# Optimization experiments

Measured on AMD Instinct MI355X. Metric: run time of the kernel, lower is better.

Reference implementation:

```python
import jax, jax.numpy as jnp
import numpy as np

N_WORDS = 100000
N_DIMS = 128
N = 65536
K = 10


def setup_inputs() -> dict:
    key = jax.random.key(0)
    k1, k2, k3, k4, k5 = jax.random.split(key, 5)
    input_idx = jax.random.randint(k1, (N,), 0, N_WORDS)
    output_idx = jax.random.randint(k2, (N,), 0, N_WORDS)
    neg_idx = jax.random.randint(k3, (N, K), 0, N_WORDS)
    # Embedding tables initialized uniform(-1, 1) as in the torch module
    W_in = jax.random.uniform(k4, (N_WORDS, N_DIMS), jnp.float32, -1.0, 1.0)
    W_out = jax.random.uniform(k5, (N_WORDS, N_DIMS), jnp.float32, -1.0, 1.0)
    return {"input_idx": input_idx, "output_idx": output_idx, "neg_idx": neg_idx,
            "W_in": W_in, "W_out": W_out}


def reference(input_idx, output_idx, neg_idx, W_in, W_out):
    in_vecs = W_in[input_idx]            # [N, D]
    out_vecs = W_out[output_idx]         # [N, D]
    neg_vecs = W_out[neg_idx]            # [N, K, D]
    prob = jnp.einsum('nd,nd->n', in_vecs, out_vecs)          # [N]
    noise = -jnp.einsum('nd,nkd->nk', in_vecs, neg_vecs)      # [N, K]
    loss = jnp.mean(jax.nn.log_sigmoid(prob) + jax.nn.log_sigmoid(noise).sum(axis=1))
    return loss
```

## Files before the change

### kernel.cpp

```cpp
#include <hip/hip_runtime.h>
#include <hip/hip_bf16.h>


#define N_SAMPLES 65536
#define N_DIMS 128
#define K_NEG 10

__global__ void zero_out_kernel(float* out) {
    if (threadIdx.x == 0 && blockIdx.x == 0) out[0] = 0.0f;
}

__device__ __forceinline__ float log_sigmoid_fast(float x) {
    float ax = fabsf(x);
    return fminf(x, 0.0f) - __logf(1.0f + __expf(-ax));
}

__device__ __forceinline__ float dot4(float4 a, float4 b) {
    return a.x * b.x + a.y * b.y + a.z * b.z + a.w * b.w;
}

__device__ __forceinline__ float group8_reduce(float v) {
    v += __shfl_xor(v, 4);
    v += __shfl_xor(v, 2);
    v += __shfl_xor(v, 1);
    return v;
}

__global__ __launch_bounds__(256, 2) void skipgram_kernel(
        const int* __restrict__ input_idx,
        const int* __restrict__ output_idx,
        const int* __restrict__ neg_idx,
        const float* __restrict__ W_in,
        const float* __restrict__ W_out,
        float* __restrict__ out)
{
    const int g = threadIdx.x & 7;
    const int n = (blockIdx.x * blockDim.x + threadIdx.x) >> 3;

    int idx[12];
    idx[0] = input_idx[n];
    idx[1] = output_idx[n];
    #pragma unroll
    for (int k = 0; k < K_NEG; ++k) idx[2 + k] = neg_idx[n * K_NEG + k];

    const float4* __restrict__ arow = (const float4*)(W_in + (size_t)idx[0] * N_DIMS);
    float4 a0 = arow[0 * 8 + g];
    float4 a1 = arow[1 * 8 + g];
    float4 a2 = arow[2 * 8 + g];
    float4 a3 = arow[3 * 8 + g];

    float4 r[11][4];
    #pragma unroll
    for (int t = 0; t < 11; ++t) {
        const float4* __restrict__ rr =
            (const float4*)(W_out + (size_t)idx[1 + t] * N_DIMS);
        r[t][0] = rr[0 * 8 + g];
        r[t][1] = rr[1 * 8 + g];
        r[t][2] = rr[2 * 8 + g];
        r[t][3] = rr[3 * 8 + g];
    }

    __builtin_amdgcn_sched_barrier(0);

    float acc = 0.0f;
    #pragma unroll
    for (int t = 0; t < 11; ++t) {
        float d = dot4(a0, r[t][0]) + dot4(a1, r[t][1])
                + dot4(a2, r[t][2]) + dot4(a3, r[t][3]);
        d = group8_reduce(d);
        acc += log_sigmoid_fast(t == 0 ? d : -d);
    }

    __shared__ float sdata[32];
    if (g == 0) sdata[threadIdx.x >> 3] = acc;
    __syncthreads();
    if (threadIdx.x < 32) {
        float s = sdata[threadIdx.x];
        s += __shfl_xor(s, 16);
        s += __shfl_xor(s, 8);
        s += __shfl_xor(s, 4);
        s += __shfl_xor(s, 2);
        s += __shfl_xor(s, 1);
        if (threadIdx.x == 0)
            atomicAdd(out, s * (1.0f / (float)N_SAMPLES));
    }
}

extern "C" void kernel_launch(void* const* d_in, const int* in_sizes, int n_in,
                              void* d_out, int out_size, void* d_ws, size_t ws_size,
                              hipStream_t stream) {
    const int*   input_idx  = (const int*)d_in[0];
    const int*   output_idx = (const int*)d_in[1];
    const int*   neg_idx    = (const int*)d_in[2];
    const float* W_in       = (const float*)d_in[3];
    const float* W_out      = (const float*)d_in[4];
    float* out = (float*)d_out;

    zero_out_kernel<<<1, 64, 0, stream>>>(out);

    const int block = 256;
    const int grid  = N_SAMPLES / (block / 8);
    skipgram_kernel<<<grid, block, 0, stream>>>(
        input_idx, output_idx, neg_idx, W_in, W_out, out);
}
```

Baseline: 158.6 us.

## Convert W_out to bf16 in workspace and gather half-width rows

Each call now runs a pre-pass that converts the whole W_out table to bf16 in the workspace buffer, and also zeroes the output. The main kernel then gathers 256-byte bf16 rows instead of 512-byte fp32 rows and widens them in registers before the dot products. This halves the bytes moved by the random-row gather, and the smaller register footprint allows an occupancy hint of 3. The trade-off is a full streaming read and write of the table on every call, plus some loss of precision in the W_out values. A fallback keeps the original fp32 path when the workspace is too small.

Result: no change. 155.6 us (-1.9%).

```diff
diff --git a/kernel.cpp b/kernel.cpp
--- a/kernel.cpp
+++ b/kernel.cpp
@@ -5,6 +5,8 @@
 #define N_SAMPLES 65536
 #define N_DIMS 128
 #define K_NEG 10
+#define N_WORDS 100000
+#define WOUT_BF16_BYTES ((size_t)N_WORDS * N_DIMS * 2)
 
 __global__ void zero_out_kernel(float* out) {
     if (threadIdx.x == 0 && blockIdx.x == 0) out[0] = 0.0f;
@@ -26,12 +28,59 @@
     return v;
 }
 
-__global__ __launch_bounds__(256, 2) void skipgram_kernel(
+__device__ __forceinline__ unsigned int f2bf(float f) {
+    unsigned int u = __float_as_uint(f);
+    return (u + 0x7FFFu + ((u >> 16) & 1u)) >> 16;
+}
+
+__global__ __launch_bounds__(256) void convert_kernel(
+        const float* __restrict__ W_out, unsigned int* __restrict__ dst,
+        float* __restrict__ out)
+{
+    if (blockIdx.x == 0 && threadIdx.x == 0) out[0] = 0.0f;
+    const size_t total8 = (size_t)N_WORDS * N_DIMS / 8;
+    const size_t stride = (size_t)gridDim.x * blockDim.x;
+    const float4* __restrict__ src = (const float4*)W_out;
+    for (size_t i = blockIdx.x * (size_t)blockDim.x + threadIdx.x;
+         i < total8; i += stride) {
+        float4 f0 = src[2 * i];
+        float4 f1 = src[2 * i + 1];
+        uint4 p;
+        p.x = f2bf(f0.x) | (f2bf(f0.y) << 16);
+        p.y = f2bf(f0.z) | (f2bf(f0.w) << 16);
+        p.z = f2bf(f1.x) | (f2bf(f1.y) << 16);
+        p.w = f2bf(f1.z) | (f2bf(f1.w) << 16);
+        ((uint4*)dst)[i] = p;
+    }
+}
+
+__device__ __forceinline__ float bflo(unsigned int u) {
+    return __uint_as_float(u << 16);
+}
+__device__ __forceinline__ float bfhi(unsigned int u) {
+    return __uint_as_float(u & 0xFFFF0000u);
+}
+__device__ __forceinline__ float dot_row_bf16(const float4 a0, const float4 a1,
+                                              const float4 a2, const float4 a3,
+                                              const uint4 b0, const uint4 b1) {
+    float acc;
+    acc  = a0.x * bflo(b0.x); acc = fmaf(a0.y, bfhi(b0.x), acc);
+    acc  = fmaf(a0.z, bflo(b0.y), acc); acc = fmaf(a0.w, bfhi(b0.y), acc);
+    acc  = fmaf(a1.x, bflo(b0.z), acc); acc = fmaf(a1.y, bfhi(b0.z), acc);
+    acc  = fmaf(a1.z, bflo(b0.w), acc); acc = fmaf(a1.w, bfhi(b0.w), acc);
+    acc  = fmaf(a2.x, bflo(b1.x), acc); acc = fmaf(a2.y, bfhi(b1.x), acc);
+    acc  = fmaf(a2.z, bflo(b1.y), acc); acc = fmaf(a2.w, bfhi(b1.y), acc);
+    acc  = fmaf(a3.x, bflo(b1.z), acc); acc = fmaf(a3.y, bfhi(b1.z), acc);
+    acc  = fmaf(a3.z, bflo(b1.w), acc); acc = fmaf(a3.w, bfhi(b1.w), acc);
+    return acc;
+}
+
+__global__ __launch_bounds__(256, 3) void skipgram_bf16_kernel(
         const int* __restrict__ input_idx,
         const int* __restrict__ output_idx,
         const int* __restrict__ neg_idx,
         const float* __restrict__ W_in,
-        const float* __restrict__ W_out,
+        const unsigned short* __restrict__ Wo16,
         float* __restrict__ out)
 {
     const int g = threadIdx.x & 7;
@@ -44,20 +93,18 @@
     for (int k = 0; k < K_NEG; ++k) idx[2 + k] = neg_idx[n * K_NEG + k];
 
     const float4* __restrict__ arow = (const float4*)(W_in + (size_t)idx[0] * N_DIMS);
-    float4 a0 = arow[0 * 8 + g];
-    float4 a1 = arow[1 * 8 + g];
-    float4 a2 = arow[2 * 8 + g];
-    float4 a3 = arow[3 * 8 + g];
-
-    float4 r[11][4];
-    #pragma unroll
-    for (int t = 0; t < 11; ++t) {
-        const float4* __restrict__ rr =
-            (const float4*)(W_out + (size_t)idx[1 + t] * N_DIMS);
-        r[t][0] = rr[0 * 8 + g];
-        r[t][1] = rr[1 * 8 + g];
-        r[t][2] = rr[2 * 8 + g];
-        r[t][3] = rr[3 * 8 + g];
+    float4 a0 = arow[4 * g + 0];
+    float4 a1 = arow[4 * g + 1];
+    float4 a2 = arow[4 * g + 2];
+    float4 a3 = arow[4 * g + 3];
+
+    uint4 r0[11], r1[11];
+    #pragma unroll
+    for (int t = 0; t < 11; ++t) {
+        const uint4* __restrict__ rr =
+            (const uint4*)(Wo16 + (size_t)idx[1 + t] * N_DIMS + 16 * g);
+        r0[t] = rr[0];
+        r1[t] = rr[1];
     }
 
     __builtin_amdgcn_sched_barrier(0);
@@ -65,8 +112,7 @@
     float acc = 0.0f;
     #pragma unroll
     for (int t = 0; t < 11; ++t) {
-        float d = dot4(a0, r[t][0]) + dot4(a1, r[t][1])
-                + dot4(a2, r[t][2]) + dot4(a3, r[t][3]);
+        float d = dot_row_bf16(a0, a1, a2, a3, r0[t], r1[t]);
         d = group8_reduce(d);
         acc += log_sigmoid_fast(t == 0 ? d : -d);
     }
@@ -86,6 +132,65 @@
     }
 }
 
+__global__ __launch_bounds__(256, 2) void skipgram_f32_kernel(
+        const int* __restrict__ input_idx,
+        const int* __restrict__ output_idx,
+        const int* __restrict__ neg_idx,
+        const float* __restrict__ W_in,
+        const float* __restrict__ W_out,
+        float* __restrict__ out)
+{
+    const int g = threadIdx.x & 7;
+    const int n = (blockIdx.x * blockDim.x + threadIdx.x) >> 3;
+
+    int idx[12];
+    idx[0] = input_idx[n];
+    idx[1] = output_idx[n];
+    #pragma unroll
+    for (int k = 0; k < K_NEG; ++k) idx[2 + k] = neg_idx[n * K_NEG + k];
+
+    const float4* __restrict__ arow = (const float4*)(W_in + (size_t)idx[0] * N_DIMS);
+    float4 a0 = arow[0 * 8 + g];
+    float4 a1 = arow[1 * 8 + g];
+    float4 a2 = arow[2 * 8 + g];
+    float4 a3 = arow[3 * 8 + g];
+
+    float4 r[11][4];
+    #pragma unroll
+    for (int t = 0; t < 11; ++t) {
+        const float4* __restrict__ rr =
+            (const float4*)(W_out + (size_t)idx[1 + t] * N_DIMS);
+        r[t][0] = rr[0 * 8 + g];
+        r[t][1] = rr[1 * 8 + g];
+        r[t][2] = rr[2 * 8 + g];
+        r[t][3] = rr[3 * 8 + g];
+    }
+    __builtin_amdgcn_sched_barrier(0);
+
+    float acc = 0.0f;
+    #pragma unroll
+    for (int t = 0; t < 11; ++t) {
+        float d = dot4(a0, r[t][0]) + dot4(a1, r[t][1])
+                + dot4(a2, r[t][2]) + dot4(a3, r[t][3]);
+        d = group8_reduce(d);
+        acc += log_sigmoid_fast(t == 0 ? d : -d);
+    }
+
+    __shared__ float sdata[32];
+    if (g == 0) sdata[threadIdx.x >> 3] = acc;
+    __syncthreads();
+    if (threadIdx.x < 32) {
+        float s = sdata[threadIdx.x];
+        s += __shfl_xor(s, 16);
+        s += __shfl_xor(s, 8);
+        s += __shfl_xor(s, 4);
+        s += __shfl_xor(s, 2);
+        s += __shfl_xor(s, 1);
+        if (threadIdx.x == 0)
+            atomicAdd(out, s * (1.0f / (float)N_SAMPLES));
+    }
+}
+
 extern "C" void kernel_launch(void* const* d_in, const int* in_sizes, int n_in,
                               void* d_out, int out_size, void* d_ws, size_t ws_size,
                               hipStream_t stream) {
@@ -96,10 +201,18 @@
     const float* W_out      = (const float*)d_in[4];
     float* out = (float*)d_out;
 
-    zero_out_kernel<<<1, 64, 0, stream>>>(out);
-
     const int block = 256;
     const int grid  = N_SAMPLES / (block / 8);
-    skipgram_kernel<<<grid, block, 0, stream>>>(
-        input_idx, output_idx, neg_idx, W_in, W_out, out);
-}
+
+    if (ws_size >= WOUT_BF16_BYTES) {
+        unsigned int* Wo16 = (unsigned int*)d_ws;
+        convert_kernel<<<2048, 256, 0, stream>>>(W_out, Wo16, out);
+        skipgram_bf16_kernel<<<grid, block, 0, stream>>>(
+            input_idx, output_idx, neg_idx, W_in,
+            (const unsigned short*)Wo16, out);
+    } else {
+        zero_out_kernel<<<1, 64, 0, stream>>>(out);
+        skipgram_f32_kernel<<<grid, block, 0, stream>>>(
+            input_idx, output_idx, neg_idx, W_in, W_out, out);
+    }
+}
```
